# Performance work log

Measured on AMD Instinct MI355X. Metric: run time of the kernel, lower is better.

Reference implementation:

```python
import jax, jax.numpy as jnp
import numpy as np
import math

T = 0.28
EPS = 1e-06
D_MODEL = 1024
N_HEADS = 16
D_K = D_MODEL // N_HEADS


def compute_radius(t, epsilon):
    raw = math.sqrt(4.0 * t * math.log(1.0 / epsilon))
    return max(int(math.ceil(raw * 2.0)), 1)

RADIUS = compute_radius(T, EPS)  # = 8 for t=0.28, eps=1e-6
WIN = RADIUS + 1                 # causal band window: j in [i-RADIUS, i]


def setup_inputs() -> dict:
    key = jax.random.key(0)
    ks = jax.random.split(key, 5)
    B, S = 2, 4096
    x = jax.random.normal(ks[0], (B, S, D_MODEL), dtype=jnp.float32)
    scale = 1.0 / math.sqrt(D_MODEL)
    Wq = jax.random.normal(ks[1], (D_MODEL, D_MODEL), dtype=jnp.float32) * scale
    Wk = jax.random.normal(ks[2], (D_MODEL, D_MODEL), dtype=jnp.float32) * scale
    Wv = jax.random.normal(ks[3], (D_MODEL, D_MODEL), dtype=jnp.float32) * scale
    Wo = jax.random.normal(ks[4], (D_MODEL, D_MODEL), dtype=jnp.float32) * scale
    return {"x": x, "Wq": Wq, "Wk": Wk, "Wv": Wv, "Wo": Wo}


def reference(x, Wq, Wk, Wv, Wo):
    B, S, _ = x.shape

    def split_heads(h):  # (B,S,D) -> (B,H,S,dk)
        return h.reshape(B, S, N_HEADS, D_K).transpose(0, 2, 1, 3)

    q = split_heads(x @ Wq)
    k = split_heads(x @ Wk)
    v = split_heads(x @ Wv)

    # Banded causal attention: token i attends to j in [i-RADIUS, i].
    # This equals the full masked softmax in the torch reference because
    # all out-of-band / non-causal entries are -inf there.
    pos = jnp.arange(S)
    idx = pos[:, None] + jnp.arange(-RADIUS, 1)[None, :]
    valid = idx >= 0                                       # left boundary
    idx_c = jnp.clip(idx, 0, S - 1)

    k_win = k[:, :, idx_c, :]
    v_win = v[:, :, idx_c, :]

    scores = jnp.einsum('bhsd,bhswd->bhsw', q, k_win) / (2.0 * T)
    scores = jnp.where(valid[None, None, :, :], scores, -jnp.inf)
    wts = jax.nn.softmax(scores, axis=-1)
    wts = jnp.nan_to_num(wts, nan=0.0)  # diagonal always valid, but keep parity

    attn = jnp.einsum('bhsw,bhswd->bhsd', wts, v_win)      # (B,H,S,dk)
    attn = attn.transpose(0, 2, 1, 3).reshape(B, S, D_MODEL)
    return attn @ Wo
```

## Files before the change

kernel.cpp:

```cpp
#include <hip/hip_runtime.h>
#include <stdint.h>

constexpr int S_LEN = 4096;
constexpr int DM    = 1024;
constexpr int RAD   = 8;
constexpr float INV2T = 1.7857142857142858f;

constexpr int BM = 128, BN = 128, BK = 32;

typedef _Float16 h8v __attribute__((ext_vector_type(8)));
typedef float f32x4  __attribute__((ext_vector_type(4)));

static __device__ __forceinline__ void gl_lds16(const void* gp, void* lp) {
  auto g = (const __attribute__((address_space(1))) void*)(uintptr_t)gp;
  auto l = (__attribute__((address_space(3))) void*)(uint32_t)(uintptr_t)lp;
  __builtin_amdgcn_global_load_lds(g, l, 16, 0, 0);
}

__global__ __launch_bounds__(256) void sda_cast_kernel(const float* __restrict__ X,
                                                       _Float16* __restrict__ Y) {
  int i = blockIdx.x * 256 + threadIdx.x;
  const float4* x4 = (const float4*)X;
  float4 a = x4[2 * i], b = x4[2 * i + 1];
  float f[8] = {a.x, a.y, a.z, a.w, b.x, b.y, b.z, b.w};
  union { _Float16 h[8]; uint4 v; } o;
#pragma unroll
  for (int j = 0; j < 8; ++j) o.h[j] = (_Float16)f[j];
  ((uint4*)Y)[i] = o.v;
}

__global__ __launch_bounds__(256) void sda_transcast_kernel(
    const float* __restrict__ W0, const float* __restrict__ W1,
    const float* __restrict__ W2, const float* __restrict__ W3,
    _Float16* __restrict__ T0, _Float16* __restrict__ T1,
    _Float16* __restrict__ T2, _Float16* __restrict__ T3) {
  __shared__ float t[32][33];
  const float* W = blockIdx.z == 0 ? W0 : (blockIdx.z == 1 ? W1 : (blockIdx.z == 2 ? W2 : W3));
  _Float16*    T = blockIdx.z == 0 ? T0 : (blockIdx.z == 1 ? T1 : (blockIdx.z == 2 ? T2 : T3));
  int tx = threadIdx.x, ty = threadIdx.y;
  int n0 = blockIdx.x * 32, k0 = blockIdx.y * 32;
#pragma unroll
  for (int i = 0; i < 4; ++i)
    t[ty + 8 * i][tx] = W[(size_t)(k0 + ty + 8 * i) * DM + n0 + tx];
  __syncthreads();
#pragma unroll
  for (int i = 0; i < 4; ++i)
    T[(size_t)(n0 + ty + 8 * i) * DM + k0 + tx] = (_Float16)t[tx][ty + 8 * i];
}

template <bool OUTF16>
__global__ __launch_bounds__(256) void sda_gemm_swz_kernel(
    const _Float16* __restrict__ A, const _Float16* __restrict__ Bt,
    void* __restrict__ C0, void* __restrict__ C1, void* __restrict__ C2) {
  constexpr int Kd = DM;
  __shared__ __align__(16) _Float16 As[BM * BK];
  __shared__ __align__(16) _Float16 Bs[BN * BK];

  int blk = blockIdx.x;
  int xcd = blk & 7, slot = blk >> 3;
  int xt = slot >> 3, ys = slot & 7;
  int yt = (xcd << 3) | ys;
  int m0 = yt * BM, n0 = xt * BN;

  int tid = threadIdx.x, wid = tid >> 6, lane = tid & 63;
  int srow = lane >> 2;
  int schunk = (lane & 3) * 8;
  int wm = (wid >> 1) * 64, wn = (wid & 1) * 64;
  int fm = lane & 15, fk = (lane >> 4) * 8;

  f32x4 acc[4][4] = {};

  for (int kt = 0; kt < Kd / BK; ++kt) {
    if (kt) __syncthreads();
    int kk = kt * BK;
    int r0 = wid * 32;
    gl_lds16(A  + (size_t)(m0 + r0 + srow)      * Kd + kk + schunk, &As[(r0)      * BK]);
    gl_lds16(A  + (size_t)(m0 + r0 + 16 + srow) * Kd + kk + schunk, &As[(r0 + 16) * BK]);
    gl_lds16(Bt + (size_t)(n0 + r0 + srow)      * Kd + kk + schunk, &Bs[(r0)      * BK]);
    gl_lds16(Bt + (size_t)(n0 + r0 + 16 + srow) * Kd + kk + schunk, &Bs[(r0 + 16) * BK]);
    __syncthreads();

    h8v af[4], bfr[4];
#pragma unroll
    for (int i = 0; i < 4; ++i)
      af[i] = *(const h8v*)&As[(wm + i * 16 + fm) * BK + fk];
#pragma unroll
    for (int j = 0; j < 4; ++j)
      bfr[j] = *(const h8v*)&Bs[(wn + j * 16 + fm) * BK + fk];
#pragma unroll
    for (int i = 0; i < 4; ++i)
#pragma unroll
      for (int j = 0; j < 4; ++j)
        acc[i][j] = __builtin_amdgcn_mfma_f32_16x16x32_f16(af[i], bfr[j], acc[i][j], 0, 0, 0);
  }

  int which = n0 >> 10, nc = n0 & 1023;
  void* Cv = which == 0 ? C0 : (which == 1 ? C1 : C2);

  int rr = (lane >> 4) * 4, cc = lane & 15;
#pragma unroll
  for (int i = 0; i < 4; ++i)
#pragma unroll
    for (int j = 0; j < 4; ++j) {
      size_t base = (size_t)(m0 + wm + i * 16 + rr) * DM + (nc + wn + j * 16 + cc);
#pragma unroll
      for (int r = 0; r < 4; ++r) {
        float v = acc[i][j][r];
        if constexpr (OUTF16) ((_Float16*)Cv)[base + (size_t)r * DM] = (_Float16)v;
        else                  ((float*)Cv)[base + (size_t)r * DM] = v;
      }
    }
}

__global__ __launch_bounds__(256) void sda_attn_kernel(
    const _Float16* __restrict__ Q, const _Float16* __restrict__ K,
    const _Float16* __restrict__ V, _Float16* __restrict__ O) {
  constexpr int VS  = 68;
  constexpr int SCS = 81;
  __shared__ __align__(16) _Float16 qs[64 * 64];
  __shared__ __align__(16) _Float16 ks[80 * 64];
  __shared__ __align__(16) _Float16 vs[96 * VS];
  __shared__ __align__(16) float    sc[64 * SCS];
  __shared__ __align__(16) _Float16 wts[64 * 96];

  int bh = blockIdx.y, b = bh >> 4, h = bh & 15;
  int s0 = blockIdx.x * 64;
  int tid = threadIdx.x;
  size_t headoff = (size_t)b * S_LEN * DM + h * 64;

  for (int idx = tid; idx < 64 * 8; idx += 256) {
    int row = idx >> 3, ch = (idx & 7) * 8;
    *(uint4*)&qs[row * 64 + ch] =
        *(const uint4*)(Q + headoff + (size_t)(s0 + row) * DM + ch);
  }
  for (int idx = tid; idx < 72 * 8; idx += 256) {
    int row = idx >> 3, ch = (idx & 7) * 8;
    int pos = s0 - RAD + row;
    uint4 kv = make_uint4(0, 0, 0, 0), vv = make_uint4(0, 0, 0, 0);
    if (pos >= 0) {
      size_t off = headoff + (size_t)pos * DM + ch;
      kv = *(const uint4*)(K + off);
      vv = *(const uint4*)(V + off);
    }
    *(uint4*)&ks[row * 64 + ch] = kv;
    *(uint2*)&vs[row * VS + ch]     = make_uint2(vv.x, vv.y);
    *(uint2*)&vs[row * VS + ch + 4] = make_uint2(vv.z, vv.w);
  }
  if (tid < 64)
    *(uint4*)&ks[(72 + (tid >> 3)) * 64 + (tid & 7) * 8] = make_uint4(0, 0, 0, 0);
  for (int idx = tid; idx < 24 * 17; idx += 256) {
    int row = 72 + idx / 17, c = (idx % 17) * 4;
    *(uint2*)&vs[row * VS + c] = make_uint2(0, 0);
  }
  for (int idx = tid; idx < 768; idx += 256)
    ((uint4*)wts)[idx] = make_uint4(0, 0, 0, 0);
  __syncthreads();

  int wid = tid >> 6, lane = tid & 63;
  int fm = lane & 15, fkg = (lane >> 4) * 8;
  int rr = (lane >> 4) * 4, cc = lane & 15;

  {
    f32x4 accs[5] = {};
    h8v aq0 = *(const h8v*)&qs[(wid * 16 + fm) * 64 + fkg];
    h8v aq1 = *(const h8v*)&qs[(wid * 16 + fm) * 64 + 32 + fkg];
#pragma unroll
    for (int t = 0; t < 5; ++t) {
      h8v bk0 = *(const h8v*)&ks[(t * 16 + fm) * 64 + fkg];
      h8v bk1 = *(const h8v*)&ks[(t * 16 + fm) * 64 + 32 + fkg];
      accs[t] = __builtin_amdgcn_mfma_f32_16x16x32_f16(aq0, bk0, accs[t], 0, 0, 0);
      accs[t] = __builtin_amdgcn_mfma_f32_16x16x32_f16(aq1, bk1, accs[t], 0, 0, 0);
    }
#pragma unroll
    for (int t = 0; t < 5; ++t)
#pragma unroll
      for (int r = 0; r < 4; ++r)
        sc[(wid * 16 + rr + r) * SCS + t * 16 + cc] = accs[t][r];
  }
  __syncthreads();

  if (tid < 64) {
    int r = tid, s = s0 + r;
    float e[9], mx = -1e30f;
#pragma unroll
    for (int j = 0; j < 9; ++j) {
      float p = sc[r * SCS + r + j] * INV2T;
      e[j] = (s - RAD + j >= 0) ? p : -1e30f;
      mx = fmaxf(mx, e[j]);
    }
    float se = 0.f;
#pragma unroll
    for (int j = 0; j < 9; ++j) { e[j] = __expf(e[j] - mx); se += e[j]; }
    float inv = 1.f / se;
#pragma unroll
    for (int j = 0; j < 9; ++j)
      wts[r * 96 + r + j] = (_Float16)(e[j] * inv);
  }
  __syncthreads();

  f32x4 acco[4] = {};
#pragma unroll
  for (int step = 0; step < 3; ++step) {
    h8v aw = *(const h8v*)&wts[(wid * 16 + fm) * 96 + step * 32 + fkg];
    int kb = step * 32 + fkg;
#pragma unroll
    for (int t = 0; t < 4; ++t) {
      h8v bv;
#pragma unroll
      for (int j = 0; j < 8; ++j)
        bv[j] = vs[(kb + j) * VS + t * 16 + fm];
      acco[t] = __builtin_amdgcn_mfma_f32_16x16x32_f16(aw, bv, acco[t], 0, 0, 0);
    }
  }
#pragma unroll
  for (int t = 0; t < 4; ++t)
#pragma unroll
    for (int r = 0; r < 4; ++r)
      O[headoff + (size_t)(s0 + wid * 16 + rr + r) * DM + t * 16 + cc] =
          (_Float16)acco[t][r];
}

extern "C" void kernel_launch(void* const* d_in, const int* in_sizes, int n_in,
                              void* d_out, int out_size, void* d_ws, size_t ws_size,
                              hipStream_t stream) {
  (void)in_sizes; (void)n_in; (void)out_size; (void)ws_size;
  const float* x  = (const float*)d_in[0];
  const float* Wq = (const float*)d_in[1];
  const float* Wk = (const float*)d_in[2];
  const float* Wv = (const float*)d_in[3];
  const float* Wo = (const float*)d_in[4];

  char* ws = (char*)d_ws;
  const size_t MB = 1ull << 20;
  _Float16* xh    = (_Float16*)(ws + 0);
  _Float16* WqkvT = (_Float16*)(ws + 16 * MB);
  _Float16* WoT   = (_Float16*)(ws + 22 * MB);
  _Float16* Qh    = (_Float16*)(ws + 24 * MB);
  _Float16* Kh    = (_Float16*)(ws + 40 * MB);
  _Float16* Vh    = (_Float16*)(ws + 56 * MB);
  _Float16* Ah    = (_Float16*)(ws + 72 * MB);

  sda_cast_kernel<<<4096, 256, 0, stream>>>(x, xh);
  sda_transcast_kernel<<<dim3(32, 32, 4), dim3(32, 8), 0, stream>>>(
      Wq, Wk, Wv, Wo,
      WqkvT, WqkvT + (size_t)DM * DM, WqkvT + 2ull * DM * DM, WoT);

  sda_gemm_swz_kernel<true><<<1536, 256, 0, stream>>>(xh, WqkvT, Qh, Kh, Vh);
  sda_attn_kernel<<<dim3(64, 32), 256, 0, stream>>>(Qh, Kh, Vh, Ah);
  sda_gemm_swz_kernel<false><<<512, 256, 0, stream>>>(Ah, WoT, d_out, d_out, d_out);
}
```

Before: 206.2 us.

## Double GEMM K-tile with XOR-swizzled LDS and trim attention score MFMAs to band

The GEMM K tile grows from 32 to 64, which halves the number of barrier-separated iterations. An XOR swizzle is applied to both the global-to-LDS load pattern and the fragment reads to avoid LDS bank conflicts with the wider rows. In the attention kernel, each wave now computes only the two 16-column key tiles that overlap its causal band instead of all five, and scores go to a smaller per-wave buffer. This cuts wasted MFMA work and LDS usage, at the cost of more LDS per GEMM block, which may reduce occupancy.

```diff
diff --git a/kernel.cpp b/kernel.cpp
--- a/kernel.cpp
+++ b/kernel.cpp
@@ -6,7 +6,7 @@
 constexpr int RAD   = 8;
 constexpr float INV2T = 1.7857142857142858f;
 
-constexpr int BM = 128, BN = 128, BK = 32;
+constexpr int BM = 128, BN = 128, BK = 64;
 
 typedef _Float16 h8v __attribute__((ext_vector_type(8)));
 typedef float f32x4  __attribute__((ext_vector_type(4)));
@@ -63,10 +63,10 @@
   int m0 = yt * BM, n0 = xt * BN;
 
   int tid = threadIdx.x, wid = tid >> 6, lane = tid & 63;
-  int srow = lane >> 2;
-  int schunk = (lane & 3) * 8;
+  int srow = lane >> 3;
+  int sgk = ((lane & 7) ^ (srow & 7)) * 8;
   int wm = (wid >> 1) * 64, wn = (wid & 1) * 64;
-  int fm = lane & 15, fk = (lane >> 4) * 8;
+  int fm = lane & 15, fc = lane >> 4;
 
   f32x4 acc[4][4] = {};
 
@@ -74,24 +74,32 @@
     if (kt) __syncthreads();
     int kk = kt * BK;
     int r0 = wid * 32;
-    gl_lds16(A  + (size_t)(m0 + r0 + srow)      * Kd + kk + schunk, &As[(r0)      * BK]);
-    gl_lds16(A  + (size_t)(m0 + r0 + 16 + srow) * Kd + kk + schunk, &As[(r0 + 16) * BK]);
-    gl_lds16(Bt + (size_t)(n0 + r0 + srow)      * Kd + kk + schunk, &Bs[(r0)      * BK]);
-    gl_lds16(Bt + (size_t)(n0 + r0 + 16 + srow) * Kd + kk + schunk, &Bs[(r0 + 16) * BK]);
+#pragma unroll
+    for (int i = 0; i < 4; ++i) {
+      gl_lds16(A  + (size_t)(m0 + r0 + i * 8 + srow) * Kd + kk + sgk, &As[(r0 + i * 8) * BK]);
+      gl_lds16(Bt + (size_t)(n0 + r0 + i * 8 + srow) * Kd + kk + sgk, &Bs[(r0 + i * 8) * BK]);
+    }
     __syncthreads();
 
-    h8v af[4], bfr[4];
-#pragma unroll
-    for (int i = 0; i < 4; ++i)
-      af[i] = *(const h8v*)&As[(wm + i * 16 + fm) * BK + fk];
-#pragma unroll
-    for (int j = 0; j < 4; ++j)
-      bfr[j] = *(const h8v*)&Bs[(wn + j * 16 + fm) * BK + fk];
-#pragma unroll
-    for (int i = 0; i < 4; ++i)
-#pragma unroll
-      for (int j = 0; j < 4; ++j)
-        acc[i][j] = __builtin_amdgcn_mfma_f32_16x16x32_f16(af[i], bfr[j], acc[i][j], 0, 0, 0);
+#pragma unroll
+    for (int ks = 0; ks < 2; ++ks) {
+      h8v af[4], bfr[4];
+#pragma unroll
+      for (int i = 0; i < 4; ++i) {
+        int row = wm + i * 16 + fm;
+        af[i] = *(const h8v*)&As[row * BK + (((ks * 4 + fc) ^ (row & 7)) * 8)];
+      }
+#pragma unroll
+      for (int j = 0; j < 4; ++j) {
+        int row = wn + j * 16 + fm;
+        bfr[j] = *(const h8v*)&Bs[row * BK + (((ks * 4 + fc) ^ (row & 7)) * 8)];
+      }
+#pragma unroll
+      for (int i = 0; i < 4; ++i)
+#pragma unroll
+        for (int j = 0; j < 4; ++j)
+          acc[i][j] = __builtin_amdgcn_mfma_f32_16x16x32_f16(af[i], bfr[j], acc[i][j], 0, 0, 0);
+    }
   }
 
   int which = n0 >> 10, nc = n0 & 1023;
@@ -116,11 +124,10 @@
     const _Float16* __restrict__ Q, const _Float16* __restrict__ K,
     const _Float16* __restrict__ V, _Float16* __restrict__ O) {
   constexpr int VS  = 68;
-  constexpr int SCS = 81;
   __shared__ __align__(16) _Float16 qs[64 * 64];
   __shared__ __align__(16) _Float16 ks[80 * 64];
   __shared__ __align__(16) _Float16 vs[96 * VS];
-  __shared__ __align__(16) float    sc[64 * SCS];
+  __shared__ __align__(16) float    scb[4 * 16 * 33];
   __shared__ __align__(16) _Float16 wts[64 * 96];
 
   int bh = blockIdx.y, b = bh >> 4, h = bh & 15;
@@ -161,30 +168,32 @@
   int rr = (lane >> 4) * 4, cc = lane & 15;
 
   {
-    f32x4 accs[5] = {};
+    f32x4 accs[2] = {};
     h8v aq0 = *(const h8v*)&qs[(wid * 16 + fm) * 64 + fkg];
     h8v aq1 = *(const h8v*)&qs[(wid * 16 + fm) * 64 + 32 + fkg];
 #pragma unroll
-    for (int t = 0; t < 5; ++t) {
+    for (int ti = 0; ti < 2; ++ti) {
+      int t = wid + ti;
       h8v bk0 = *(const h8v*)&ks[(t * 16 + fm) * 64 + fkg];
       h8v bk1 = *(const h8v*)&ks[(t * 16 + fm) * 64 + 32 + fkg];
-      accs[t] = __builtin_amdgcn_mfma_f32_16x16x32_f16(aq0, bk0, accs[t], 0, 0, 0);
-      accs[t] = __builtin_amdgcn_mfma_f32_16x16x32_f16(aq1, bk1, accs[t], 0, 0, 0);
-    }
-#pragma unroll
-    for (int t = 0; t < 5; ++t)
+      accs[ti] = __builtin_amdgcn_mfma_f32_16x16x32_f16(aq0, bk0, accs[ti], 0, 0, 0);
+      accs[ti] = __builtin_amdgcn_mfma_f32_16x16x32_f16(aq1, bk1, accs[ti], 0, 0, 0);
+    }
+#pragma unroll
+    for (int ti = 0; ti < 2; ++ti)
 #pragma unroll
       for (int r = 0; r < 4; ++r)
-        sc[(wid * 16 + rr + r) * SCS + t * 16 + cc] = accs[t][r];
+        scb[wid * 528 + (rr + r) * 33 + ti * 16 + cc] = accs[ti][r];
   }
   __syncthreads();
 
   if (tid < 64) {
     int r = tid, s = s0 + r;
+    const float* my = &scb[(r >> 4) * 528 + (r & 15) * 33 + (r & 15)];
     float e[9], mx = -1e30f;
 #pragma unroll
     for (int j = 0; j < 9; ++j) {
-      float p = sc[r * SCS + r + j] * INV2T;
+      float p = my[j] * INV2T;
       e[j] = (s - RAD + j >= 0) ? p : -1e30f;
       mx = fmaxf(mx, e[j]);
     }
```

New measurement: 190.2 us. -7.7%, faster.
